# Performance work log

Hardware: AMD Instinct MI355X
Metric: run time of the kernel (lower is better)

## Reference

```python
import jax, jax.numpy as jnp
import numpy as np
from jax import lax

EPS = 1e-6  # matches nn.CosineSimilarity(eps=1e-6)


def _box_sum_3x3(z):
    # z: [B,1,H,W] -> 3x3 same-padded box sum (kernel of ones)
    k = jnp.ones((1, 1, 3, 3), z.dtype)
    return lax.conv_general_dilated(z, k, (1, 1), ((1, 1), (1, 1)),
                                    dimension_numbers=('NCHW', 'OIHW', 'NCHW'))


def setup_inputs() -> dict:
    key = jax.random.key(0)
    k1, k2 = jax.random.split(key)
    T, B, C, H, W = 4, 32, 256, 32, 32
    x = jax.random.normal(k1, (T, B, C, H, W), dtype=jnp.float32)
    prev_drop_mask = jax.random.bernoulli(k2, 0.3, (B, H * W))
    return {"x": x, "prev_drop_mask": prev_drop_mask}


def reference(x, prev_drop_mask):
    T, B, C, H, W = x.shape
    xm = jnp.mean(x, axis=0)                      # [B,C,H,W]
    # F.conv2d with ones(C,C,3,3)/9 gives an output identical across output
    # channels: box3x3(sum_c x) / 9. Compute that single channel exactly.
    csum = jnp.sum(xm, axis=1, keepdims=True)     # [B,1,H,W]
    lm = _box_sum_3x3(csum) / 9.0                 # [B,1,H,W] == local_mean[:,o] for every o
    lm = lm.reshape(B, H * W)                     # [B,P]
    xf = xm.reshape(B, C, H * W)                  # [B,C,P]
    # cosine over channel dim; local_mean vector is lm replicated C times:
    #   dot = lm * sum_c x,  ||lm_vec|| = sqrt(C)*|lm|
    dot = lm * csum.reshape(B, H * W)
    nx = jnp.linalg.norm(xf, axis=1)              # [B,P]
    ny = jnp.sqrt(jnp.asarray(C, xm.dtype)) * jnp.abs(lm)
    sim = dot / (jnp.maximum(nx, EPS) * jnp.maximum(ny, EPS))
    scores = jnp.where(prev_drop_mask, -jnp.inf, -sim)
    return jax.nn.softmax(scores, axis=1).reshape(B, H, W)
```

## Files before the change

kernel.cpp:

```cpp
#include <hip/hip_runtime.h>
#include <math.h>

#define Bv 32
#define Cv 256
#define Hv 32
#define Wv 32
#define Pv 1024
#define Tv 4
#define TSTRIDE (Bv * Cv * Pv)

__global__ __launch_bounds__(256) void lss_partial(
    const float* __restrict__ x,
    float* __restrict__ part1,
    float* __restrict__ part2,
    int cc)
{
    const int chunk = blockIdx.x;
    const int b     = blockIdx.y;
    const int tid   = threadIdx.x;
    const int p4    = tid << 2;
    const int c0    = chunk * cc;

    float s1x = 0.f, s1y = 0.f, s1z = 0.f, s1w = 0.f;
    float s2x = 0.f, s2y = 0.f, s2z = 0.f, s2w = 0.f;

    const float* bp = x + ((size_t)b * Cv + c0) * Pv + p4;

    #pragma unroll 4
    for (int c = 0; c < cc; ++c) {
        const float4 v0 = *(const float4*)(bp);
        const float4 v1 = *(const float4*)(bp + (size_t)TSTRIDE);
        const float4 v2 = *(const float4*)(bp + (size_t)2 * TSTRIDE);
        const float4 v3 = *(const float4*)(bp + (size_t)3 * TSTRIDE);
        bp += Pv;

        const float mx = (v0.x + v1.x + v2.x + v3.x) * 0.25f;
        const float my = (v0.y + v1.y + v2.y + v3.y) * 0.25f;
        const float mz = (v0.z + v1.z + v2.z + v3.z) * 0.25f;
        const float mw = (v0.w + v1.w + v2.w + v3.w) * 0.25f;

        s1x += mx;  s2x += mx * mx;
        s1y += my;  s2y += my * my;
        s1z += mz;  s2z += mz * mz;
        s1w += mw;  s2w += mw * mw;
    }

    const size_t o = ((size_t)chunk * Bv + b) * Pv + p4;
    float4 r1; r1.x = s1x; r1.y = s1y; r1.z = s1z; r1.w = s1w;
    float4 r2; r2.x = s2x; r2.y = s2y; r2.z = s2z; r2.w = s2w;
    *(float4*)(part1 + o) = r1;
    *(float4*)(part2 + o) = r2;
}

__global__ __launch_bounds__(1024) void lss_final(
    const float* __restrict__ part1,
    const float* __restrict__ part2,
    const int*   __restrict__ mask,
    float*       __restrict__ out,
    int nch)
{
    const int b   = blockIdx.x;
    const int tid = threadIdx.x;
    const int yy  = tid >> 5;
    const int xx  = tid & 31;

    __shared__ float cs[(Hv + 2) * (Wv + 2)];
    __shared__ float red[Pv];

    float s1 = 0.f, s2 = 0.f;
    for (int ch = 0; ch < nch; ++ch) {
        const size_t o = ((size_t)ch * Bv + b) * Pv + tid;
        s1 += part1[o];
        s2 += part2[o];
    }
    const float csum = s1;
    const float nx   = sqrtf(s2);

    for (int i = tid; i < (Hv + 2) * (Wv + 2); i += Pv) cs[i] = 0.f;
    __syncthreads();
    cs[(yy + 1) * (Wv + 2) + (xx + 1)] = csum;
    __syncthreads();

    float lm = 0.f;
    #pragma unroll
    for (int dy = 0; dy < 3; ++dy)
        #pragma unroll
        for (int dx = 0; dx < 3; ++dx)
            lm += cs[(yy + dy) * (Wv + 2) + (xx + dx)];
    lm *= (1.0f / 9.0f);

    const float ny  = 16.0f * fabsf(lm);
    const float sim = (lm * csum) / (fmaxf(nx, 1e-6f) * fmaxf(ny, 1e-6f));

    const float score = mask[b * Pv + tid] ? -INFINITY : -sim;

    red[tid] = score;
    __syncthreads();
    for (int s = Pv / 2; s > 0; s >>= 1) {
        if (tid < s) red[tid] = fmaxf(red[tid], red[tid + s]);
        __syncthreads();
    }
    const float m = red[0];
    __syncthreads();

    const float e = expf(score - m);
    red[tid] = e;
    __syncthreads();
    for (int s = Pv / 2; s > 0; s >>= 1) {
        if (tid < s) red[tid] += red[tid + s];
        __syncthreads();
    }
    const float denom = red[0];

    out[b * Pv + tid] = e / denom;
}

extern "C" void kernel_launch(void* const* d_in, const int* in_sizes, int n_in,
                              void* d_out, int out_size, void* d_ws, size_t ws_size,
                              hipStream_t stream) {
    const float* x    = (const float*)d_in[0];
    const int*   mask = (const int*)d_in[1];
    float*       out  = (float*)d_out;

    int nch = 16;
    while (nch > 1 && (size_t)nch * Bv * Pv * 2 * sizeof(float) > ws_size) nch >>= 1;
    const int cc = Cv / nch;

    float* part1 = (float*)d_ws;
    float* part2 = part1 + (size_t)nch * Bv * Pv;

    dim3 g1(nch, Bv);
    lss_partial<<<g1, 256, 0, stream>>>(x, part1, part2, cc);
    lss_final<<<Bv, Pv, 0, stream>>>(part1, part2, mask, out, nch);
}
```

Before: 196.9 us.

## Split partial reduction into mid kernel, raise chunk count, use wave shuffles for softmax

Doubles the channel chunk count so the first pass launches more blocks. Adds a separate mid kernel that sums the per-chunk partials across 256 blocks, instead of leaving that sum to 32 large blocks in the final kernel. The final kernel's softmax max and sum reductions now use 64-wide wave shuffles plus a 16-entry shared array, replacing the tree of shared-memory barriers. The cost is an extra kernel launch and a round trip through global memory for the intermediate sums.

```diff
diff --git a/kernel.cpp b/kernel.cpp
--- a/kernel.cpp
+++ b/kernel.cpp
@@ -52,29 +52,43 @@
     *(float4*)(part2 + o) = r2;
 }
 
-__global__ __launch_bounds__(1024) void lss_final(
+__global__ __launch_bounds__(128) void lss_mid(
     const float* __restrict__ part1,
     const float* __restrict__ part2,
+    float* __restrict__ csum_o,
+    float* __restrict__ nx_o,
+    int nch)
+{
+    const int b = blockIdx.y;
+    const int p = blockIdx.x * 128 + threadIdx.x;
+
+    float s1 = 0.f, s2 = 0.f;
+    for (int ch = 0; ch < nch; ++ch) {
+        const size_t o = ((size_t)ch * Bv + b) * Pv + p;
+        s1 += part1[o];
+        s2 += part2[o];
+    }
+    csum_o[b * Pv + p] = s1;
+    nx_o[b * Pv + p]   = sqrtf(s2);
+}
+
+__global__ __launch_bounds__(1024) void lss_final(
+    const float* __restrict__ csum_i,
+    const float* __restrict__ nx_i,
     const int*   __restrict__ mask,
-    float*       __restrict__ out,
-    int nch)
+    float*       __restrict__ out)
 {
     const int b   = blockIdx.x;
     const int tid = threadIdx.x;
     const int yy  = tid >> 5;
     const int xx  = tid & 31;
+    const int wid = tid >> 6;
 
     __shared__ float cs[(Hv + 2) * (Wv + 2)];
-    __shared__ float red[Pv];
+    __shared__ float wred[16];
 
-    float s1 = 0.f, s2 = 0.f;
-    for (int ch = 0; ch < nch; ++ch) {
-        const size_t o = ((size_t)ch * Bv + b) * Pv + tid;
-        s1 += part1[o];
-        s2 += part2[o];
-    }
-    const float csum = s1;
-    const float nx   = sqrtf(s2);
+    const float csum = csum_i[b * Pv + tid];
+    const float nx   = nx_i[b * Pv + tid];
 
     for (int i = tid; i < (Hv + 2) * (Wv + 2); i += Pv) cs[i] = 0.f;
     __syncthreads();
@@ -94,23 +108,28 @@
 
     const float score = mask[b * Pv + tid] ? -INFINITY : -sim;
 
-    red[tid] = score;
+    float v = score;
+    #pragma unroll
+    for (int off = 32; off > 0; off >>= 1)
+        v = fmaxf(v, __shfl_xor(v, off, 64));
+    if ((tid & 63) == 0) wred[wid] = v;
     __syncthreads();
-    for (int s = Pv / 2; s > 0; s >>= 1) {
-        if (tid < s) red[tid] = fmaxf(red[tid], red[tid + s]);
-        __syncthreads();
-    }
-    const float m = red[0];
+    float m = wred[0];
+    #pragma unroll
+    for (int i = 1; i < 16; ++i) m = fmaxf(m, wred[i]);
     __syncthreads();
 
     const float e = expf(score - m);
-    red[tid] = e;
+
+    v = e;
+    #pragma unroll
+    for (int off = 32; off > 0; off >>= 1)
+        v += __shfl_xor(v, off, 64);
+    if ((tid & 63) == 0) wred[wid] = v;
     __syncthreads();
-    for (int s = Pv / 2; s > 0; s >>= 1) {
-        if (tid < s) red[tid] += red[tid + s];
-        __syncthreads();
-    }
-    const float denom = red[0];
+    float denom = 0.f;
+    #pragma unroll
+    for (int i = 0; i < 16; ++i) denom += wred[i];
 
     out[b * Pv + tid] = e / denom;
 }
@@ -122,14 +141,20 @@
     const int*   mask = (const int*)d_in[1];
     float*       out  = (float*)d_out;
 
-    int nch = 16;
-    while (nch > 1 && (size_t)nch * Bv * Pv * 2 * sizeof(float) > ws_size) nch >>= 1;
+    int nch = 32;
+    while (nch > 1 &&
+           ((size_t)nch * Bv * Pv * 2 + 2 * (size_t)Bv * Pv) * sizeof(float) > ws_size)
+        nch >>= 1;
     const int cc = Cv / nch;
 
-    float* part1 = (float*)d_ws;
-    float* part2 = part1 + (size_t)nch * Bv * Pv;
+    float* part1  = (float*)d_ws;
+    float* part2  = part1 + (size_t)nch * Bv * Pv;
+    float* csum_b = part2 + (size_t)nch * Bv * Pv;
+    float* nx_b   = csum_b + (size_t)Bv * Pv;
 
     dim3 g1(nch, Bv);
     lss_partial<<<g1, 256, 0, stream>>>(x, part1, part2, cc);
-    lss_final<<<Bv, Pv, 0, stream>>>(part1, part2, mask, out, nch);
+    dim3 g2(Pv / 128, Bv);
+    lss_mid<<<g2, 128, 0, stream>>>(part1, part2, csum_b, nx_b, nch);
+    lss_final<<<Bv, Pv, 0, stream>>>(csum_b, nx_b, mask, out);
 }
```

New measurement: 200.9 us. +2.0%, slower.

## Fuse partial reduction and softmax via last-block atomic counter

Applied to the files above, without the earlier changes.

Merges the two kernels into one. The last block to finish for each batch, detected with an atomic counter, performs the channel reduction, box filter and softmax. The finalize step now handles four pixels per thread and uses wavefront shuffles instead of a shared-memory tree. This removes a kernel launch and the serialized tail kernel, but adds a memset launch and assumes the workspace is large enough for 16 chunks plus the counters.

```diff
diff --git a/kernel.cpp b/kernel.cpp
--- a/kernel.cpp
+++ b/kernel.cpp
@@ -6,113 +6,134 @@
 #define Hv 32
 #define Wv 32
 #define Pv 1024
-#define Tv 4
 #define TSTRIDE (Bv * Cv * Pv)
+#define NCH 16
+#define CC  (Cv / NCH)
 
-__global__ __launch_bounds__(256) void lss_partial(
+__global__ __launch_bounds__(256) void lss_fused(
     const float* __restrict__ x,
-    float* __restrict__ part1,
-    float* __restrict__ part2,
-    int cc)
+    const int*   __restrict__ mask,
+    float*       __restrict__ out,
+    float*       __restrict__ part1,
+    float*       __restrict__ part2,
+    int*         __restrict__ cnt)
 {
     const int chunk = blockIdx.x;
     const int b     = blockIdx.y;
     const int tid   = threadIdx.x;
     const int p4    = tid << 2;
-    const int c0    = chunk * cc;
 
-    float s1x = 0.f, s1y = 0.f, s1z = 0.f, s1w = 0.f;
-    float s2x = 0.f, s2y = 0.f, s2z = 0.f, s2w = 0.f;
+    {
+        float s1x = 0.f, s1y = 0.f, s1z = 0.f, s1w = 0.f;
+        float s2x = 0.f, s2y = 0.f, s2z = 0.f, s2w = 0.f;
 
-    const float* bp = x + ((size_t)b * Cv + c0) * Pv + p4;
+        const float* bp = x + ((size_t)b * Cv + chunk * CC) * Pv + p4;
 
-    #pragma unroll 4
-    for (int c = 0; c < cc; ++c) {
-        const float4 v0 = *(const float4*)(bp);
-        const float4 v1 = *(const float4*)(bp + (size_t)TSTRIDE);
-        const float4 v2 = *(const float4*)(bp + (size_t)2 * TSTRIDE);
-        const float4 v3 = *(const float4*)(bp + (size_t)3 * TSTRIDE);
-        bp += Pv;
+        #pragma unroll 4
+        for (int c = 0; c < CC; ++c) {
+            const float4 v0 = *(const float4*)(bp);
+            const float4 v1 = *(const float4*)(bp + (size_t)TSTRIDE);
+            const float4 v2 = *(const float4*)(bp + (size_t)2 * TSTRIDE);
+            const float4 v3 = *(const float4*)(bp + (size_t)3 * TSTRIDE);
+            bp += Pv;
 
-        const float mx = (v0.x + v1.x + v2.x + v3.x) * 0.25f;
-        const float my = (v0.y + v1.y + v2.y + v3.y) * 0.25f;
-        const float mz = (v0.z + v1.z + v2.z + v3.z) * 0.25f;
-        const float mw = (v0.w + v1.w + v2.w + v3.w) * 0.25f;
+            const float mx = (v0.x + v1.x + v2.x + v3.x) * 0.25f;
+            const float my = (v0.y + v1.y + v2.y + v3.y) * 0.25f;
+            const float mz = (v0.z + v1.z + v2.z + v3.z) * 0.25f;
+            const float mw = (v0.w + v1.w + v2.w + v3.w) * 0.25f;
 
-        s1x += mx;  s2x += mx * mx;
-        s1y += my;  s2y += my * my;
-        s1z += mz;  s2z += mz * mz;
-        s1w += mw;  s2w += mw * mw;
+            s1x += mx;  s2x += mx * mx;
+            s1y += my;  s2y += my * my;
+            s1z += mz;  s2z += mz * mz;
+            s1w += mw;  s2w += mw * mw;
+        }
+
+        const size_t o = ((size_t)chunk * Bv + b) * Pv + p4;
+        float4 r1; r1.x = s1x; r1.y = s1y; r1.z = s1z; r1.w = s1w;
+        float4 r2; r2.x = s2x; r2.y = s2y; r2.z = s2z; r2.w = s2w;
+        *(float4*)(part1 + o) = r1;
+        *(float4*)(part2 + o) = r2;
     }
 
-    const size_t o = ((size_t)chunk * Bv + b) * Pv + p4;
-    float4 r1; r1.x = s1x; r1.y = s1y; r1.z = s1z; r1.w = s1w;
-    float4 r2; r2.x = s2x; r2.y = s2y; r2.z = s2z; r2.w = s2w;
-    *(float4*)(part1 + o) = r1;
-    *(float4*)(part2 + o) = r2;
-}
-
-__global__ __launch_bounds__(1024) void lss_final(
-    const float* __restrict__ part1,
-    const float* __restrict__ part2,
-    const int*   __restrict__ mask,
-    float*       __restrict__ out,
-    int nch)
-{
-    const int b   = blockIdx.x;
-    const int tid = threadIdx.x;
-    const int yy  = tid >> 5;
-    const int xx  = tid & 31;
+    __shared__ int s_last;
+    if (tid == 0) {
+        __threadfence();
+        s_last = (atomicAdd(&cnt[b], 1) == NCH - 1);
+    }
+    __syncthreads();
+    if (!s_last) return;
+    __threadfence();
 
     __shared__ float cs[(Hv + 2) * (Wv + 2)];
-    __shared__ float red[Pv];
+    __shared__ float wred[4];
 
-    float s1 = 0.f, s2 = 0.f;
-    for (int ch = 0; ch < nch; ++ch) {
-        const size_t o = ((size_t)ch * Bv + b) * Pv + tid;
-        s1 += part1[o];
-        s2 += part2[o];
+    float c0 = 0.f, c1 = 0.f, c2 = 0.f, c3 = 0.f;
+    float q0 = 0.f, q1 = 0.f, q2 = 0.f, q3 = 0.f;
+    #pragma unroll
+    for (int ch = 0; ch < NCH; ++ch) {
+        const size_t o = ((size_t)ch * Bv + b) * Pv + p4;
+        const float4 a = *(const float4*)(part1 + o);
+        const float4 s = *(const float4*)(part2 + o);
+        c0 += a.x; c1 += a.y; c2 += a.z; c3 += a.w;
+        q0 += s.x; q1 += s.y; q2 += s.z; q3 += s.w;
     }
-    const float csum = s1;
-    const float nx   = sqrtf(s2);
+    const float nx0 = sqrtf(q0), nx1 = sqrtf(q1), nx2 = sqrtf(q2), nx3 = sqrtf(q3);
 
-    for (int i = tid; i < (Hv + 2) * (Wv + 2); i += Pv) cs[i] = 0.f;
+    for (int i = tid; i < (Hv + 2) * (Wv + 2); i += 256) cs[i] = 0.f;
     __syncthreads();
-    cs[(yy + 1) * (Wv + 2) + (xx + 1)] = csum;
+    const int yy  = tid >> 3;
+    const int xx0 = (tid & 7) << 2;
+    float* crow = &cs[(yy + 1) * (Wv + 2) + (xx0 + 1)];
+    crow[0] = c0; crow[1] = c1; crow[2] = c2; crow[3] = c3;
     __syncthreads();
 
-    float lm = 0.f;
+    float lm0 = 0.f, lm1 = 0.f, lm2 = 0.f, lm3 = 0.f;
     #pragma unroll
-    for (int dy = 0; dy < 3; ++dy)
-        #pragma unroll
-        for (int dx = 0; dx < 3; ++dx)
-            lm += cs[(yy + dy) * (Wv + 2) + (xx + dx)];
-    lm *= (1.0f / 9.0f);
+    for (int dy = 0; dy < 3; ++dy) {
+        const float* r = &cs[(yy + dy) * (Wv + 2) + xx0];
+        const float r0 = r[0], r1 = r[1], r2 = r[2], r3 = r[3], r4 = r[4], r5 = r[5];
+        lm0 += r0 + r1 + r2;
+        lm1 += r1 + r2 + r3;
+        lm2 += r2 + r3 + r4;
+        lm3 += r3 + r4 + r5;
+    }
+    lm0 *= (1.0f / 9.0f); lm1 *= (1.0f / 9.0f);
+    lm2 *= (1.0f / 9.0f); lm3 *= (1.0f / 9.0f);
 
-    const float ny  = 16.0f * fabsf(lm);
-    const float sim = (lm * csum) / (fmaxf(nx, 1e-6f) * fmaxf(ny, 1e-6f));
+    const float sim0 = (lm0 * c0) / (fmaxf(nx0, 1e-6f) * fmaxf(16.0f * fabsf(lm0), 1e-6f));
+    const float sim1 = (lm1 * c1) / (fmaxf(nx1, 1e-6f) * fmaxf(16.0f * fabsf(lm1), 1e-6f));
+    const float sim2 = (lm2 * c2) / (fmaxf(nx2, 1e-6f) * fmaxf(16.0f * fabsf(lm2), 1e-6f));
+    const float sim3 = (lm3 * c3) / (fmaxf(nx3, 1e-6f) * fmaxf(16.0f * fabsf(lm3), 1e-6f));
 
-    const float score = mask[b * Pv + tid] ? -INFINITY : -sim;
+    const int4 mk = *(const int4*)(mask + b * Pv + p4);
+    float sc0 = mk.x ? -INFINITY : -sim0;
+    float sc1 = mk.y ? -INFINITY : -sim1;
+    float sc2 = mk.z ? -INFINITY : -sim2;
+    float sc3 = mk.w ? -INFINITY : -sim3;
 
-    red[tid] = score;
+    const int wid = tid >> 6;
+    float v = fmaxf(fmaxf(sc0, sc1), fmaxf(sc2, sc3));
+    #pragma unroll
+    for (int off = 32; off > 0; off >>= 1)
+        v = fmaxf(v, __shfl_xor(v, off, 64));
+    if ((tid & 63) == 0) wred[wid] = v;
     __syncthreads();
-    for (int s = Pv / 2; s > 0; s >>= 1) {
-        if (tid < s) red[tid] = fmaxf(red[tid], red[tid + s]);
-        __syncthreads();
-    }
-    const float m = red[0];
+    const float m = fmaxf(fmaxf(wred[0], wred[1]), fmaxf(wred[2], wred[3]));
     __syncthreads();
 
-    const float e = expf(score - m);
-    red[tid] = e;
+    const float e0 = expf(sc0 - m), e1 = expf(sc1 - m);
+    const float e2 = expf(sc2 - m), e3 = expf(sc3 - m);
+
+    v = (e0 + e1) + (e2 + e3);
+    #pragma unroll
+    for (int off = 32; off > 0; off >>= 1)
+        v += __shfl_xor(v, off, 64);
+    if ((tid & 63) == 0) wred[wid] = v;
     __syncthreads();
-    for (int s = Pv / 2; s > 0; s >>= 1) {
-        if (tid < s) red[tid] += red[tid + s];
-        __syncthreads();
-    }
-    const float denom = red[0];
+    const float inv = 1.0f / (((wred[0] + wred[1]) + (wred[2] + wred[3])));
 
-    out[b * Pv + tid] = e / denom;
+    float4 r; r.x = e0 * inv; r.y = e1 * inv; r.z = e2 * inv; r.w = e3 * inv;
+    *(float4*)(out + b * Pv + p4) = r;
 }
 
 extern "C" void kernel_launch(void* const* d_in, const int* in_sizes, int n_in,
@@ -122,14 +143,12 @@
     const int*   mask = (const int*)d_in[1];
     float*       out  = (float*)d_out;
 
-    int nch = 16;
-    while (nch > 1 && (size_t)nch * Bv * Pv * 2 * sizeof(float) > ws_size) nch >>= 1;
-    const int cc = Cv / nch;
+    float* part1 = (float*)d_ws;
+    float* part2 = part1 + (size_t)NCH * Bv * Pv;
+    int*   cnt   = (int*)(part2 + (size_t)NCH * Bv * Pv);
 
-    float* part1 = (float*)d_ws;
-    float* part2 = part1 + (size_t)nch * Bv * Pv;
+    hipMemsetAsync(cnt, 0, Bv * sizeof(int), stream);
 
-    dim3 g1(nch, Bv);
-    lss_partial<<<g1, 256, 0, stream>>>(x, part1, part2, cc);
-    lss_final<<<Bv, Pv, 0, stream>>>(part1, part2, mask, out, nch);
+    dim3 grid(NCH, Bv);
+    lss_fused<<<grid, 256, 0, stream>>>(x, mask, out, part1, part2, cnt);
 }
```

Measured after the change: 234.4 us. +19.0%, slower.
